# Kernel optimization log

Measured on AMD Instinct MI355X. Metric: run time of the kernel, lower is better.

The kernel has to match this reference:

```python
import jax, jax.numpy as jnp
import numpy as np

B, L, D, K, NFFT = 4, 8192, 768, 24, 16384


def setup_inputs() -> dict:
    key = jax.random.key(0)
    k1, k2, k3, k4 = jax.random.split(key, 4)
    x = jax.random.normal(k1, (B, L, D), dtype=jnp.float32)
    phi = jax.random.normal(k2, (L, K), dtype=jnp.float32) * 0.1
    M_inputs = jax.random.normal(k3, (D, D), dtype=jnp.float32) * 0.02
    M_filters = jax.random.normal(k4, (K, D), dtype=jnp.float32) * 0.02
    return {"x": x, "phi": phi, "M_inputs": M_inputs, "M_filters": M_filters, "n": NFFT}


def _convolve_approx(u, v, n):
    # u: (B, L, D) projected inputs; v: (L, D) projected filters (per-channel kernels)
    bsz, seq_len, d = u.shape
    sgn = jnp.where(jnp.arange(seq_len) % 2 == 0, 1.0, -1.0).astype(u.dtype)[None, :, None]  # (1,L,1)
    V = jnp.fft.rfft(v.astype(jnp.float32), n=n, axis=0)[None, :, :, None]  # (1,F,D,1)
    U = jnp.stack([u, u * sgn], axis=-1).astype(jnp.float32)  # (B,L,D,2): [plus, sign-flipped]
    Uf = jnp.fft.rfft(U, n=n, axis=1)  # (B,F,D,2)
    conv = jnp.fft.irfft(V * Uf, n=n, axis=1)[:, :seq_len]  # (B,L,D,2)
    U_plus = conv[..., 0]
    U_minus = conv[..., 1] * sgn
    return U_plus, U_minus


def reference(x, phi, M_inputs, M_filters, n):
    x_proj = x @ M_inputs          # (B,L,D)
    phi_proj = phi @ M_filters     # (L,D)
    spectral_plus, spectral_minus = _convolve_approx(x_proj, phi_proj, n)
    return spectral_plus + spectral_minus
```

## Files before the change

kernel.cpp:

```cpp
#include <hip/hip_runtime.h>
#include <stdint.h>

#define B_SZ 4
#define L_SEQ 8192
#define D_CH 768
#define K_F 24
#define NFFT2 8192
#define LDS_BYTES 69632

typedef __attribute__((ext_vector_type(4))) float f32x4;
typedef __attribute__((ext_vector_type(8))) __bf16 bf16x8;

__device__ __forceinline__ uint32_t f2bf1(float f) {
  uint32_t u = __float_as_uint(f);
  return (u + 0x7fffu + ((u >> 16) & 1u)) >> 16;
}
__device__ __forceinline__ uint32_t packbf2(float lo, float hi) {
  return f2bf1(lo) | (f2bf1(hi) << 16);
}
__device__ __forceinline__ float2 unpackbf2(uint32_t v) {
  return float2{__uint_as_float(v << 16), __uint_as_float(v & 0xffff0000u)};
}
__device__ __forceinline__ float2 cmulf(float2 a, float2 b) {
  return float2{a.x * b.x - a.y * b.y, a.x * b.y + a.y * b.x};
}
__device__ __forceinline__ uint32_t pkbf(float lo, float hi) {
  uint32_t r;
  asm("v_cvt_pk_bf16_f32 %0, %1, %2" : "=v"(r) : "v"(lo), "v"(hi));
  return r;
}

__global__ __launch_bounds__(256) void k_mit(const float* __restrict__ Mi,
                                             uint16_t* __restrict__ MiT) {
  int i = blockIdx.x * 256 + threadIdx.x;
  int n = i / 768, e = i - n * 768;
  MiT[i] = (uint16_t)f2bf1(Mi[e * 768 + n]);
}

template <int S>
__device__ __forceinline__ void dft8(float2* x) {
  const float C = 0.70710678118654752f;
  float2 t0{x[0].x + x[4].x, x[0].y + x[4].y}, t1{x[0].x - x[4].x, x[0].y - x[4].y};
  float2 t2{x[2].x + x[6].x, x[2].y + x[6].y}, t3{x[2].x - x[6].x, x[2].y - x[6].y};
  float2 t4{x[1].x + x[5].x, x[1].y + x[5].y}, t5{x[1].x - x[5].x, x[1].y - x[5].y};
  float2 t6{x[3].x + x[7].x, x[3].y + x[7].y}, t7{x[3].x - x[7].x, x[3].y - x[7].y};
  float2 t3r = (S < 0) ? float2{t3.y, -t3.x} : float2{-t3.y, t3.x};
  float2 t7r = (S < 0) ? float2{t7.y, -t7.x} : float2{-t7.y, t7.x};
  float2 e0{t0.x + t2.x, t0.y + t2.y}, e2{t0.x - t2.x, t0.y - t2.y};
  float2 e1{t1.x + t3r.x, t1.y + t3r.y}, e3{t1.x - t3r.x, t1.y - t3r.y};
  float2 o0{t4.x + t6.x, t4.y + t6.y}, o2{t4.x - t6.x, t4.y - t6.y};
  float2 o1{t5.x + t7r.x, t5.y + t7r.y}, o3{t5.x - t7r.x, t5.y - t7r.y};
  float2 o1r = (S < 0) ? float2{C * (o1.x + o1.y), C * (o1.y - o1.x)}
                       : float2{C * (o1.x - o1.y), C * (o1.y + o1.x)};
  float2 o2r = (S < 0) ? float2{o2.y, -o2.x} : float2{-o2.y, o2.x};
  float2 o3r = (S < 0) ? float2{C * (o3.y - o3.x), -C * (o3.x + o3.y)}
                       : float2{-C * (o3.x + o3.y), C * (o3.x - o3.y)};
  x[0] = float2{e0.x + o0.x, e0.y + o0.y};
  x[4] = float2{e0.x - o0.x, e0.y - o0.y};
  x[1] = float2{e1.x + o1r.x, e1.y + o1r.y};
  x[5] = float2{e1.x - o1r.x, e1.y - o1r.y};
  x[2] = float2{e2.x + o2r.x, e2.y + o2r.y};
  x[6] = float2{e2.x - o2r.x, e2.y - o2r.y};
  x[3] = float2{e3.x + o3r.x, e3.y + o3r.y};
  x[7] = float2{e3.x - o3r.x, e3.y - o3r.y};
}

template <int LH, int S, int NT>
__device__ __forceinline__ void pass_r8(float2* a, int tid) {
  constexpr int h = 1 << LH;
  constexpr int st = h + (h >> 4);
  const float ang = (S < 0 ? -6.2831853071795864769f : 6.2831853071795864769f) / (float)(h * 8);
  __syncthreads();
#pragma unroll
  for (int jj = 0; jj < 1024 / NT; ++jj) {
    int j = jj * NT + tid;
    int pos = j & (h - 1);
    int base = ((j >> LH) << (LH + 3)) + pos;
    float2* p = a + (base + (base >> 4));
    float2 x[8];
#pragma unroll
    for (int q = 0; q < 8; ++q) x[q] = p[q * st];
    float sn, cs;
    __sincosf(ang * (float)pos, &sn, &cs);
    float2 w{cs, sn};
    if constexpr (S < 0) {
      dft8<-1>(x);
      float2 wq = w;
      x[1] = cmulf(x[1], wq);
#pragma unroll
      for (int q = 2; q < 8; ++q) {
        wq = cmulf(wq, w);
        x[q] = cmulf(x[q], wq);
      }
    } else {
      float2 wq = w;
      x[1] = cmulf(x[1], wq);
#pragma unroll
      for (int q = 2; q < 8; ++q) {
        wq = cmulf(wq, w);
        x[q] = cmulf(x[q], wq);
      }
      dft8<1>(x);
    }
#pragma unroll
    for (int q = 0; q < 8; ++q) p[q * st] = x[q];
  }
}

__device__ __forceinline__ void p1_fused(float2* a, const uint32_t* __restrict__ row32, int tid) {
#pragma unroll
  for (int jj = 0; jj < 2; ++jj) {
    int j = jj * 512 + tid;
    float2 x[8];
#pragma unroll
    for (int q = 0; q < 4; ++q) x[q] = unpackbf2(row32[j + q * 1024]);
    x[4] = x[5] = x[6] = x[7] = float2{0.f, 0.f};
    dft8<-1>(x);
    float sn, cs;
    __sincosf(-6.2831853071795864769f / 8192.0f * (float)j, &sn, &cs);
    float2 w{cs, sn}, wq = w;
    x[1] = cmulf(x[1], wq);
#pragma unroll
    for (int q = 2; q < 8; ++q) {
      wq = cmulf(wq, w);
      x[q] = cmulf(x[q], wq);
    }
    float2* p = a + (j + (j >> 4));
#pragma unroll
    for (int q = 0; q < 8; ++q) p[q * 1088] = x[q];
  }
}

__device__ __forceinline__ void mid_fused(float2* a, const uint32_t* __restrict__ wrow, int tid) {
  __syncthreads();
#pragma unroll
  for (int jj = 0; jj < 8; ++jj) {
    int j = jj * 512 + tid;
    float2* p = a + (2 * j + ((2 * j) >> 4));
    float2 u = p[0], v = p[1];
    float2 s{u.x + v.x, u.y + v.y}, dd{u.x - v.x, u.y - v.y};
    uint2 wv = *(const uint2*)(wrow + 2 * j);
    s = cmulf(s, unpackbf2(wv.x));
    dd = cmulf(dd, unpackbf2(wv.y));
    p[0] = float2{s.x + dd.x, s.y + dd.y};
    p[1] = float2{s.x - dd.x, s.y - dd.y};
  }
}

__device__ __forceinline__ void last_fused(float2* a, uint32_t* __restrict__ out32, int tid) {
  __syncthreads();
#pragma unroll
  for (int jj = 0; jj < 2; ++jj) {
    int j = jj * 512 + tid;
    float2* p = a + (j + (j >> 4));
    float2 x[8];
#pragma unroll
    for (int q = 0; q < 8; ++q) x[q] = p[q * 1088];
    float sn, cs;
    __sincosf(6.2831853071795864769f / 8192.0f * (float)j, &sn, &cs);
    float2 w{cs, sn}, wq = w;
    x[1] = cmulf(x[1], wq);
#pragma unroll
    for (int q = 2; q < 8; ++q) {
      wq = cmulf(wq, w);
      x[q] = cmulf(x[q], wq);
    }
    dft8<1>(x);
#pragma unroll
    for (int q = 0; q < 4; ++q) out32[j + q * 1024] = packbf2(x[q].x, x[q].y);
  }
}

__global__ __launch_bounds__(256) void k_phi(const float* __restrict__ phi,
                                             float2* __restrict__ Phi2) {
  extern __shared__ float2 buf[];
  int k = blockIdx.x, tid = threadIdx.x;
  const float scale = 2.0f / 8192.0f;
  for (int r = tid; r < 4096; r += 256) {
    buf[r + (r >> 4)] = float2{phi[(2 * r) * K_F + k] * scale, 0.0f};
    int r2i = r + 4096;
    buf[r2i + (r2i >> 4)] = float2{0.0f, 0.0f};
  }
  pass_r8<10, -1, 256>(buf, tid);
  pass_r8<7, -1, 256>(buf, tid);
  pass_r8<4, -1, 256>(buf, tid);
  pass_r8<1, -1, 256>(buf, tid);
  __syncthreads();
  for (int j = tid; j < 4096; j += 256) {
    float2* p = buf + (2 * j + ((2 * j) >> 4));
    float2 u = p[0], v = p[1];
    p[0] = float2{u.x + v.x, u.y + v.y};
    p[1] = float2{u.x - v.x, u.y - v.y};
  }
  __syncthreads();
  for (int f = tid; f < NFFT2; f += 256) Phi2[k * NFFT2 + f] = buf[f + (f >> 4)];
}

__global__ __launch_bounds__(256) void k_w2(const float2* __restrict__ Phi2,
                                            const float* __restrict__ Mf,
                                            uint32_t* __restrict__ W2) {
  __shared__ float2 p[K_F][256];
  __shared__ float mf[K_F][32];
  int tid = threadIdx.x;
  int fc = blockIdx.x & 31, dc = blockIdx.x >> 5;
  int f0 = fc * 256, d0 = dc * 32;
  for (int i = tid; i < K_F * 256; i += 256) {
    int k = i >> 8, fl = i & 255;
    p[k][fl] = Phi2[k * NFFT2 + f0 + fl];
  }
  for (int i = tid; i < K_F * 32; i += 256) {
    int k = i >> 5, dl = i & 31;
    mf[k][dl] = Mf[k * D_CH + d0 + dl];
  }
  __syncthreads();
  for (int dl = 0; dl < 32; ++dl) {
    float re = 0.f, im = 0.f;
#pragma unroll
    for (int k = 0; k < K_F; ++k) {
      float m = mf[k][dl];
      re += m * p[k][tid].x;
      im += m * p[k][tid].y;
    }
    W2[(size_t)(d0 + dl) * NFFT2 + f0 + tid] = packbf2(re, im);
  }
}

__device__ __forceinline__ void gload_lds16(const void* g, void* l) {
  __builtin_amdgcn_global_load_lds(
      (const __attribute__((address_space(1))) void*)g,
      (__attribute__((address_space(3))) void*)l, 16, 0, 0);
}

__global__ __launch_bounds__(256) void k_gemm(const float* __restrict__ X,
                                              const uint16_t* __restrict__ MiT,
                                              uint16_t* __restrict__ Cp) {
  __shared__ uint16_t As[128 * 64];
  __shared__ uint16_t Bs[128 * 64];
  int tid = threadIdx.x;
  int lane = tid & 63, wid = tid >> 6;
  int bm = blockIdx.x / 6, bn = blockIdx.x % 6;
  int m0 = bm * 128, n0 = bn * 128;
  int wr = wid >> 1, wc = wid & 1;
  int lm = lane & 15, lg = lane >> 4;
  f32x4 acc[4][4] = {};

  for (int kt = 0; kt < 12; ++kt) {
    int k0 = kt * 64;
    __syncthreads();
#pragma unroll
    for (int it = 0; it < 4; ++it) {
      int s = it * 256 + tid;
      int row = s >> 3;
      int cb = ((s & 7) << 4) ^ ((row & 7) << 4);
      gload_lds16(MiT + (size_t)(n0 + row) * 768 + k0 + (cb >> 1),
                  (char*)Bs + (it * 256 + wid * 64) * 16);
    }
#pragma unroll
    for (int it = 0; it < 4; ++it) {
      int s = it * 256 + tid;
      int row = s >> 3, c16 = s & 7;
      const float* src = X + (size_t)(m0 + row) * 768 + k0 + c16 * 8;
      float4 f0 = *(const float4*)src;
      float4 f1 = *(const float4*)(src + 4);
      uint4 o;
      o.x = pkbf(f0.x, f0.y);
      o.y = pkbf(f0.z, f0.w);
      o.z = pkbf(f1.x, f1.y);
      o.w = pkbf(f1.z, f1.w);
      *(uint4*)((char*)As + row * 128 + ((c16 << 4) ^ ((row & 7) << 4))) = o;
    }
    asm volatile("s_waitcnt vmcnt(0)" ::: "memory");
    __syncthreads();
#pragma unroll
    for (int ks = 0; ks < 2; ++ks) {
      int kbyte = (ks * 32 + lg * 8) * 2;
      bf16x8 a[4], b[4];
#pragma unroll
      for (int mi = 0; mi < 4; ++mi) {
        int row = wr * 64 + mi * 16 + lm;
        a[mi] = *(const bf16x8*)((const char*)As + row * 128 + (kbyte ^ ((row & 7) << 4)));
      }
#pragma unroll
      for (int ni = 0; ni < 4; ++ni) {
        int row = wc * 64 + ni * 16 + lm;
        b[ni] = *(const bf16x8*)((const char*)Bs + row * 128 + (kbyte ^ ((row & 7) << 4)));
      }
#pragma unroll
      for (int mi = 0; mi < 4; ++mi)
#pragma unroll
        for (int ni = 0; ni < 4; ++ni)
          acc[mi][ni] = __builtin_amdgcn_mfma_f32_16x16x32_bf16(a[mi], b[ni], acc[mi][ni], 0, 0, 0);
    }
  }
#pragma unroll
  for (int mi = 0; mi < 4; ++mi) {
#pragma unroll
    for (int ni = 0; ni < 4; ++ni) {
      int mg = m0 + wr * 64 + mi * 16 + lg * 4;
      int dd = n0 + wc * 64 + ni * 16 + lm;
      int bb = mg >> 13, t = mg & 8191;
      f32x4 v = acc[mi][ni];
      uint2 o;
      o.x = packbf2(v[0], v[1]);
      o.y = packbf2(v[2], v[3]);
      *(uint2*)(Cp + ((size_t)bb * 768 + dd) * 8192 + t) = o;
    }
  }
}

__global__ __launch_bounds__(512, 4) void k_conv(const uint16_t* __restrict__ xprojT,
                                                 const uint32_t* __restrict__ W2,
                                                 uint16_t* __restrict__ convo) {
  extern __shared__ float2 buf[];
  int tid = threadIdx.x;
  int bd = blockIdx.x;
  int d = bd % 768;
  const uint32_t* row32 = (const uint32_t*)(xprojT + (size_t)bd * 8192);
  p1_fused(buf, row32, tid);
  pass_r8<7, -1, 512>(buf, tid);
  pass_r8<4, -1, 512>(buf, tid);
  pass_r8<1, -1, 512>(buf, tid);
  mid_fused(buf, W2 + (size_t)d * NFFT2, tid);
  pass_r8<1, 1, 512>(buf, tid);
  pass_r8<4, 1, 512>(buf, tid);
  pass_r8<7, 1, 512>(buf, tid);
  last_fused(buf, (uint32_t*)(convo + (size_t)bd * 8192), tid);
}

__global__ __launch_bounds__(256) void k_tr(const uint16_t* __restrict__ convo,
                                            float* __restrict__ out) {
  __shared__ uint16_t tile[64][72];
  int tid = threadIdx.x;
  int bx = blockIdx.x;
  int b = bx / 1536;
  int r = bx - b * 1536;
  int d0 = (r >> 7) << 6;
  int t0 = (r & 127) << 6;
  {
    int rr = tid >> 3;
    int c8 = (tid & 7) << 3;
#pragma unroll
    for (int p = 0; p < 2; ++p) {
      int row = p * 32 + rr;
      uint4 v = *(const uint4*)(convo + ((size_t)(b * 768 + d0 + row)) * 8192 + t0 + c8);
      *(uint4*)&tile[row][c8] = v;
    }
  }
  __syncthreads();
  {
    int c4 = (tid & 15) << 2;
    int tg = tid >> 4;
#pragma unroll
    for (int p = 0; p < 4; ++p) {
      int tt = p * 16 + tg;
      float4 o;
      o.x = __uint_as_float((uint32_t)tile[c4 + 0][tt] << 16);
      o.y = __uint_as_float((uint32_t)tile[c4 + 1][tt] << 16);
      o.z = __uint_as_float((uint32_t)tile[c4 + 2][tt] << 16);
      o.w = __uint_as_float((uint32_t)tile[c4 + 3][tt] << 16);
      *(float4*)(out + ((size_t)b * 8192 + t0 + tt) * 768 + d0 + c4) = o;
    }
  }
}

extern "C" void kernel_launch(void* const* d_in, const int* in_sizes, int n_in,
                              void* d_out, int out_size, void* d_ws, size_t ws_size,
                              hipStream_t stream) {
  const float* x   = (const float*)d_in[0];
  const float* phi = (const float*)d_in[1];
  const float* Mi  = (const float*)d_in[2];
  const float* Mf  = (const float*)d_in[3];
  float* out = (float*)d_out;

  uint16_t* xprojT = (uint16_t*)d_out + 25165824;

  char* ws = (char*)d_ws;
  uint16_t* convo = (uint16_t*)ws;
  uint32_t* W2    = (uint32_t*)(ws + 50331648);
  float2*   Phi2  = (float2*)(ws + 75497472);
  uint16_t* MiT   = (uint16_t*)(ws + 77070336);

  k_mit<<<2304, 256, 0, stream>>>(Mi, MiT);
  k_phi<<<24, 256, LDS_BYTES, stream>>>(phi, Phi2);
  k_w2<<<768, 256, 0, stream>>>(Phi2, Mf, W2);
  k_gemm<<<1536, 256, 0, stream>>>(x, MiT, xprojT);
  k_conv<<<3072, 512, LDS_BYTES, stream>>>(xprojT, W2, convo);
  k_tr<<<6144, 256, 0, stream>>>(convo, out);
}
```

Baseline: 253.2 us.

## Restructure projection GEMM around resident B panel and fuse conv middle stages

The GEMM now keeps a 96-column slice of the bf16 weight matrix resident in LDS for the whole K range. Each wave streams its own 64 rows of X straight from global memory into registers, converting them to bf16 on the fly. This removes the per-K-tile A staging and the barriers, and a blockIdx swizzle is added for cache locality. Separately, the conv kernel merges the last forward radix-8 pass, the pointwise filter multiply and the first inverse pass into one register-resident 16-point routine, which removes two LDS round trips and two barriers. The risks are uncoalesced direct A loads, a 147KB LDS footprint that limits occupancy, and higher register pressure.

```diff
diff --git a/kernel.cpp b/kernel.cpp
--- a/kernel.cpp
+++ b/kernel.cpp
@@ -7,6 +7,7 @@
 #define K_F 24
 #define NFFT2 8192
 #define LDS_BYTES 69632
+#define GEMM_LDS 147456
 
 typedef __attribute__((ext_vector_type(4))) float f32x4;
 typedef __attribute__((ext_vector_type(8))) __bf16 bf16x8;
@@ -131,19 +132,53 @@
   }
 }
 
-__device__ __forceinline__ void mid_fused(float2* a, const uint32_t* __restrict__ wrow, int tid) {
-  __syncthreads();
-#pragma unroll
-  for (int jj = 0; jj < 8; ++jj) {
-    int j = jj * 512 + tid;
-    float2* p = a + (2 * j + ((2 * j) >> 4));
-    float2 u = p[0], v = p[1];
-    float2 s{u.x + v.x, u.y + v.y}, dd{u.x - v.x, u.y - v.y};
-    uint2 wv = *(const uint2*)(wrow + 2 * j);
-    s = cmulf(s, unpackbf2(wv.x));
-    dd = cmulf(dd, unpackbf2(wv.y));
-    p[0] = float2{s.x + dd.x, s.y + dd.y};
-    p[1] = float2{s.x - dd.x, s.y - dd.y};
+__device__ __forceinline__ void mid16(float2* a, const uint32_t* __restrict__ wrow, int tid) {
+  const float C1 = 0.92387953251128675613f, S1 = 0.38268343236508977173f;
+  const float C2 = 0.70710678118654752440f;
+  __syncthreads();
+  int m = tid;
+  float2* p = a + 17 * m;
+  float2 e[8], o[8];
+#pragma unroll
+  for (int q = 0; q < 8; ++q) {
+    e[q] = p[2 * q];
+    o[q] = p[2 * q + 1];
+  }
+  dft8<-1>(e);
+  dft8<-1>(o);
+  o[1] = cmulf(o[1], float2{C1, -S1});
+  o[2] = cmulf(o[2], float2{C2, -C2});
+  o[3] = cmulf(o[3], float2{S1, -C1});
+  o[4] = float2{o[4].y, -o[4].x};
+  o[5] = cmulf(o[5], float2{-S1, -C1});
+  o[6] = cmulf(o[6], float2{-C2, -C2});
+  o[7] = cmulf(o[7], float2{-C1, -S1});
+  const uint4* wp = (const uint4*)(wrow + 16 * m);
+  uint4 w0 = wp[0], w1 = wp[1], w2 = wp[2], w3 = wp[3];
+  uint32_t wv[16] = {w0.x, w0.y, w0.z, w0.w, w1.x, w1.y, w1.z, w1.w,
+                     w2.x, w2.y, w2.z, w2.w, w3.x, w3.y, w3.z, w3.w};
+#pragma unroll
+  for (int q = 0; q < 8; ++q) {
+    float2 s{e[q].x + o[q].x, e[q].y + o[q].y};
+    float2 d{e[q].x - o[q].x, e[q].y - o[q].y};
+    s = cmulf(s, unpackbf2(wv[2 * q]));
+    d = cmulf(d, unpackbf2(wv[2 * q + 1]));
+    e[q] = float2{s.x + d.x, s.y + d.y};
+    o[q] = float2{s.x - d.x, s.y - d.y};
+  }
+  o[1] = cmulf(o[1], float2{C1, S1});
+  o[2] = cmulf(o[2], float2{C2, C2});
+  o[3] = cmulf(o[3], float2{S1, C1});
+  o[4] = float2{-o[4].y, o[4].x};
+  o[5] = cmulf(o[5], float2{-S1, C1});
+  o[6] = cmulf(o[6], float2{-C2, C2});
+  o[7] = cmulf(o[7], float2{-C1, S1});
+  dft8<1>(e);
+  dft8<1>(o);
+#pragma unroll
+  for (int q = 0; q < 8; ++q) {
+    p[2 * q] = e[q];
+    p[2 * q + 1] = o[q];
   }
 }
 
@@ -231,78 +266,70 @@
       (__attribute__((address_space(3))) void*)l, 16, 0, 0);
 }
 
-__global__ __launch_bounds__(256) void k_gemm(const float* __restrict__ X,
-                                              const uint16_t* __restrict__ MiT,
-                                              uint16_t* __restrict__ Cp) {
-  __shared__ uint16_t As[128 * 64];
-  __shared__ uint16_t Bs[128 * 64];
+__global__ __launch_bounds__(512, 2) void k_gemm(const float* __restrict__ X,
+                                                 const uint16_t* __restrict__ MiT,
+                                                 uint16_t* __restrict__ Cp) {
+  extern __shared__ char lds[];
   int tid = threadIdx.x;
   int lane = tid & 63, wid = tid >> 6;
-  int bm = blockIdx.x / 6, bn = blockIdx.x % 6;
-  int m0 = bm * 128, n0 = bn * 128;
-  int wr = wid >> 1, wc = wid & 1;
+  int pb = blockIdx.x;
+  int v = (pb & 7) * 64 + (pb >> 3);
+  int bm = v / 8, bn = v % 8;
+  int m0 = bm * 512 + wid * 64;
+  int n0 = bn * 96;
   int lm = lane & 15, lg = lane >> 4;
-  f32x4 acc[4][4] = {};
-
-  for (int kt = 0; kt < 12; ++kt) {
-    int k0 = kt * 64;
-    __syncthreads();
-#pragma unroll
-    for (int it = 0; it < 4; ++it) {
-      int s = it * 256 + tid;
-      int row = s >> 3;
-      int cb = ((s & 7) << 4) ^ ((row & 7) << 4);
-      gload_lds16(MiT + (size_t)(n0 + row) * 768 + k0 + (cb >> 1),
-                  (char*)Bs + (it * 256 + wid * 64) * 16);
-    }
-#pragma unroll
-    for (int it = 0; it < 4; ++it) {
-      int s = it * 256 + tid;
-      int row = s >> 3, c16 = s & 7;
-      const float* src = X + (size_t)(m0 + row) * 768 + k0 + c16 * 8;
+
+#pragma unroll
+  for (int it = 0; it < 18; ++it) {
+    int s = it * 512 + tid;
+    int row = s / 96, c16 = s - row * 96;
+    int csw = c16 ^ (row & 7);
+    gload_lds16(MiT + (size_t)(n0 + row) * 768 + csw * 8,
+                lds + (it * 512 + wid * 64) * 16);
+  }
+  asm volatile("s_waitcnt vmcnt(0)" ::: "memory");
+  __syncthreads();
+
+  f32x4 acc[4][6] = {};
+#pragma unroll
+  for (int ks = 0; ks < 24; ++ks) {
+    bf16x8 a[4], b[6];
+#pragma unroll
+    for (int mi = 0; mi < 4; ++mi) {
+      const float* src = X + (size_t)(m0 + mi * 16 + lm) * 768 + ks * 32 + lg * 8;
       float4 f0 = *(const float4*)src;
       float4 f1 = *(const float4*)(src + 4);
-      uint4 o;
-      o.x = pkbf(f0.x, f0.y);
-      o.y = pkbf(f0.z, f0.w);
-      o.z = pkbf(f1.x, f1.y);
-      o.w = pkbf(f1.z, f1.w);
-      *(uint4*)((char*)As + row * 128 + ((c16 << 4) ^ ((row & 7) << 4))) = o;
-    }
-    asm volatile("s_waitcnt vmcnt(0)" ::: "memory");
-    __syncthreads();
-#pragma unroll
-    for (int ks = 0; ks < 2; ++ks) {
-      int kbyte = (ks * 32 + lg * 8) * 2;
-      bf16x8 a[4], b[4];
-#pragma unroll
-      for (int mi = 0; mi < 4; ++mi) {
-        int row = wr * 64 + mi * 16 + lm;
-        a[mi] = *(const bf16x8*)((const char*)As + row * 128 + (kbyte ^ ((row & 7) << 4)));
-      }
-#pragma unroll
-      for (int ni = 0; ni < 4; ++ni) {
-        int row = wc * 64 + ni * 16 + lm;
-        b[ni] = *(const bf16x8*)((const char*)Bs + row * 128 + (kbyte ^ ((row & 7) << 4)));
-      }
-#pragma unroll
-      for (int mi = 0; mi < 4; ++mi)
-#pragma unroll
-        for (int ni = 0; ni < 4; ++ni)
-          acc[mi][ni] = __builtin_amdgcn_mfma_f32_16x16x32_bf16(a[mi], b[ni], acc[mi][ni], 0, 0, 0);
-    }
-  }
+      uint4 u;
+      u.x = pkbf(f0.x, f0.y);
+      u.y = pkbf(f0.z, f0.w);
+      u.z = pkbf(f1.x, f1.y);
+      u.w = pkbf(f1.z, f1.w);
+      a[mi] = *(const bf16x8*)&u;
+    }
+#pragma unroll
+    for (int ni = 0; ni < 6; ++ni) {
+      int row_l = ni * 16 + lm;
+      int c16 = (ks * 4 + lg) ^ (row_l & 7);
+      b[ni] = *(const bf16x8*)(lds + row_l * 1536 + c16 * 16);
+    }
+#pragma unroll
+    for (int mi = 0; mi < 4; ++mi)
+#pragma unroll
+      for (int ni = 0; ni < 6; ++ni)
+        acc[mi][ni] = __builtin_amdgcn_mfma_f32_16x16x32_bf16(a[mi], b[ni], acc[mi][ni], 0, 0, 0);
+  }
+
 #pragma unroll
   for (int mi = 0; mi < 4; ++mi) {
 #pragma unroll
-    for (int ni = 0; ni < 4; ++ni) {
-      int mg = m0 + wr * 64 + mi * 16 + lg * 4;
-      int dd = n0 + wc * 64 + ni * 16 + lm;
+    for (int ni = 0; ni < 6; ++ni) {
+      int mg = m0 + mi * 16 + lg * 4;
+      int dd = n0 + ni * 16 + lm;
       int bb = mg >> 13, t = mg & 8191;
-      f32x4 v = acc[mi][ni];
+      f32x4 vv = acc[mi][ni];
       uint2 o;
-      o.x = packbf2(v[0], v[1]);
-      o.y = packbf2(v[2], v[3]);
+      o.x = packbf2(vv[0], vv[1]);
+      o.y = packbf2(vv[2], vv[3]);
       *(uint2*)(Cp + ((size_t)bb * 768 + dd) * 8192 + t) = o;
     }
   }
@@ -319,9 +346,7 @@
   p1_fused(buf, row32, tid);
   pass_r8<7, -1, 512>(buf, tid);
   pass_r8<4, -1, 512>(buf, tid);
-  pass_r8<1, -1, 512>(buf, tid);
-  mid_fused(buf, W2 + (size_t)d * NFFT2, tid);
-  pass_r8<1, 1, 512>(buf, tid);
+  mid16(buf, W2 + (size_t)d * NFFT2, tid);
   pass_r8<4, 1, 512>(buf, tid);
   pass_r8<7, 1, 512>(buf, tid);
   last_fused(buf, (uint32_t*)(convo + (size_t)bd * 8192), tid);
@@ -383,7 +408,7 @@
   k_mit<<<2304, 256, 0, stream>>>(Mi, MiT);
   k_phi<<<24, 256, LDS_BYTES, stream>>>(phi, Phi2);
   k_w2<<<768, 256, 0, stream>>>(Phi2, Mf, W2);
-  k_gemm<<<1536, 256, 0, stream>>>(x, MiT, xprojT);
+  k_gemm<<<512, 512, GEMM_LDS, stream>>>(x, MiT, xprojT);
   k_conv<<<3072, 512, LDS_BYTES, stream>>>(xprojT, W2, convo);
   k_tr<<<6144, 256, 0, stream>>>(convo, out);
 }
```

New measurement: 282.0 us. 11.4% more time.
